# Performance work log

Measured on AMD Instinct MI355X. Metric: run time of the kernel, lower is better.

## Reference

```python
import jax, jax.numpy as jnp
import numpy as np

B, T, D = 4, 2048, 1024
N_HEAD, HEAD_SIZE = 16, 64
MASK_FILL = 1e-9  # faithful to original: masked_fill uses 1e-9, not -inf


def setup_inputs() -> dict:
    key = jax.random.key(0)
    k1, k2, k3 = jax.random.split(key, 3)
    x = jax.random.normal(k1, (B, T, D), dtype=jnp.float32)
    # per-head qkv projection weights, stacked: [n_head, d_model, 3*head_size]
    W_qkv = jax.random.normal(k2, (N_HEAD, D, 3 * HEAD_SIZE), dtype=jnp.float32) * (D ** -0.5)
    # output projection [d_model, d_model] (x @ W_out convention)
    W_out = jax.random.normal(k3, (D, D), dtype=jnp.float32) * (D ** -0.5)
    return {"x": x, "W_qkv": W_qkv, "W_out": W_out}


def reference(x, W_qkv, W_out):
    Bv, Tv, C = x.shape
    # qkv for all heads at once: [B, H, T, 3*head_size]
    qkv = jnp.einsum("btc,hcf->bhtf", x, W_qkv)
    q, k, v = jnp.split(qkv, 3, axis=-1)  # each [B, H, T, head_size]
    # NOTE: original scales by C**-0.5 where C = d_model (not head_size)
    scores = jnp.einsum("bhtd,bhsd->bhts", q, k) * (C ** -0.5)
    causal = jnp.tril(jnp.ones((Tv, Tv), dtype=bool))
    # faithful bug: masked positions set to 1e-9 before softmax (not -inf)
    scores = jnp.where(causal, scores, MASK_FILL)
    attn = jax.nn.softmax(scores, axis=-1)
    out_heads = jnp.einsum("bhts,bhsd->bhtd", attn, v)  # [B, H, T, head_size]
    mha = out_heads.transpose(0, 2, 1, 3).reshape(Bv, Tv, C)  # concat heads
    return mha @ W_out
```

## Files before the change

### kernel.cpp

```cpp
#include <hip/hip_runtime.h>

typedef unsigned short u16;
typedef __attribute__((ext_vector_type(8))) short short8;
typedef __attribute__((ext_vector_type(4))) short short4v;
typedef __attribute__((ext_vector_type(4))) float f32x4;

#define B_  4
#define T_  2048
#define D_  1024
#define H_  16
#define HS_ 64
#define M_    (B_ * T_)
#define NQKV_ (H_ * 3 * HS_)
#define NTILE_ (T_ / 64)
#define LOG2E_ 1.44269504088896340736f

__device__ __forceinline__ u16 f2bf(float f) {
  union { float f; unsigned u; } v; v.f = f;
  unsigned u = v.u;
  return (u16)((u + 0x7FFFu + ((u >> 16) & 1u)) >> 16);
}
__device__ __forceinline__ float bf2f(u16 h) {
  union { unsigned u; float f; } v; v.u = ((unsigned)h) << 16; return v.f;
}
__device__ __forceinline__ unsigned pkbf(float lo, float hi) {
  unsigned r;
  asm("v_cvt_pk_bf16_f32 %0, %1, %2" : "=v"(r) : "v"(lo), "v"(hi));
  return r;
}
__device__ __forceinline__ float exp2fast(float x) {
  float r;
  asm("v_exp_f32 %0, %1" : "=v"(r) : "v"(x));
  return r;
}
__device__ __forceinline__ void gload16(const u16* g, u16* l) {
  __builtin_amdgcn_global_load_lds(
      (const __attribute__((address_space(1))) void*)g,
      (__attribute__((address_space(3))) void*)l, 16, 0, 0);
}

__global__ void k_cvt_x(const float* __restrict__ x, u16* __restrict__ o, int n4) {
  int i = blockIdx.x * 256 + threadIdx.x;
  if (i < n4) {
    float4 v = ((const float4*)x)[i];
    short4v d;
    d[0] = (short)f2bf(v.x); d[1] = (short)f2bf(v.y);
    d[2] = (short)f2bf(v.z); d[3] = (short)f2bf(v.w);
    ((short4v*)o)[i] = d;
  }
}

__global__ void k_transpose_cvt(const float* __restrict__ in, u16* __restrict__ out,
                                int R, int C, long sIn, long sOut) {
  __shared__ float tile[32][33];
  int h = blockIdx.z;
  const float* src = in + (long)h * sIn;
  u16* dst = out + (long)h * sOut;
  int r0 = blockIdx.y * 32, c0 = blockIdx.x * 32;
  int tx = threadIdx.x, ty = threadIdx.y;
  #pragma unroll
  for (int i = 0; i < 32; i += 8) {
    int r = r0 + ty + i, c = c0 + tx;
    tile[ty + i][tx] = (r < R && c < C) ? src[(long)r * C + c] : 0.f;
  }
  __syncthreads();
  #pragma unroll
  for (int i = 0; i < 32; i += 8) {
    int c = c0 + ty + i, r = r0 + tx;
    if (c < C && r < R) dst[(long)c * R + r] = f2bf(tile[tx][ty + i]);
  }
}

template<int MODE>
__global__ __launch_bounds__(256) void k_gemm(
    const u16* __restrict__ A, const u16* __restrict__ Bt,
    u16* __restrict__ Oq, u16* __restrict__ Ok, u16* __restrict__ Ov,
    float* __restrict__ Of, int K) {
  __shared__ __align__(16) u16 As[128 * 32];
  __shared__ __align__(16) u16 Bs[128 * 32];
  int mt = blockIdx.x, nt = blockIdx.y;
  int tid = threadIdx.x;
  int wid = tid >> 6, lane = tid & 63;
  int lr = lane & 15, lg = lane >> 4;
  int mw = (wid >> 1) * 64, nw = (wid & 1) * 64;
  int c0chunk = wid * 128 + lane;
  int row0 = c0chunk >> 2,      q0 = c0chunk & 3;
  int row1 = (c0chunk + 64) >> 2, q1 = (c0chunk + 64) & 3;
  const u16* Arow0 = A  + (long)(mt * 128 + row0) * K + q0 * 8;
  const u16* Arow1 = A  + (long)(mt * 128 + row1) * K + q1 * 8;
  const u16* Brow0 = Bt + (long)(nt * 128 + row0) * K + q0 * 8;
  const u16* Brow1 = Bt + (long)(nt * 128 + row1) * K + q1 * 8;
  u16* ldsA0 = As + (wid * 128) * 8;
  u16* ldsA1 = As + (wid * 128 + 64) * 8;
  u16* ldsB0 = Bs + (wid * 128) * 8;
  u16* ldsB1 = Bs + (wid * 128 + 64) * 8;
  f32x4 acc[4][4] = {};
  for (int k0 = 0; k0 < K; k0 += 32) {
    __syncthreads();
    gload16(Arow0 + k0, ldsA0);
    gload16(Arow1 + k0, ldsA1);
    gload16(Brow0 + k0, ldsB0);
    gload16(Brow1 + k0, ldsB1);
    __syncthreads();
    short8 af[4], bf[4];
    #pragma unroll
    for (int i = 0; i < 4; i++)
      af[i] = *(const short8*)(As + (mw + i * 16 + lr) * 32 + lg * 8);
    #pragma unroll
    for (int i = 0; i < 4; i++)
      bf[i] = *(const short8*)(Bs + (nw + i * 16 + lr) * 32 + lg * 8);
    #pragma unroll
    for (int i = 0; i < 4; i++)
      #pragma unroll
      for (int j = 0; j < 4; j++)
        acc[i][j] = __builtin_amdgcn_mfma_f32_16x16x32_bf16(af[i], bf[j], acc[i][j], 0, 0, 0);
  }
  if constexpr (MODE == 0) {
    __shared__ __align__(16) u16 Cs[128 * 128];
    #pragma unroll
    for (int j = 0; j < 4; j++) {
      int fbase = (nt * 128 + nw + j * 16) % 192;
      float sc = (fbase < 64) ? (0.03125f * LOG2E_) : 1.0f;
      #pragma unroll
      for (int i = 0; i < 4; i++) {
        int row = mw + i * 16 + lg * 4;
        int col = nw + j * 16 + lr;
        #pragma unroll
        for (int r = 0; r < 4; r++)
          Cs[(row + r) * 128 + col] = f2bf(acc[i][j][r] * sc);
      }
    }
    __syncthreads();
    #pragma unroll
    for (int p5 = 0; p5 < 8; p5++) {
      int idx = p5 * 2048 + tid * 8;
      int row = idx >> 7, col = idx & 127;
      short8 v = *(const short8*)(Cs + row * 128 + col);
      int m = mt * 128 + row;
      int n0 = nt * 128 + col;
      int b = m >> 11, t = m & (T_ - 1);
      int h = n0 / 192, f = n0 % 192;
      long o = (((long)(b * H_ + h)) * T_ + t) * HS_;
      u16* dst = (f < 64) ? (Oq + o + f) : (f < 128) ? (Ok + o + f - 64) : (Ov + o + f - 128);
      *(short8*)dst = v;
    }
  } else {
    #pragma unroll
    for (int i = 0; i < 4; i++) {
      #pragma unroll
      for (int j = 0; j < 4; j++) {
        int mbase = mt * 128 + mw + i * 16 + lg * 4;
        int n     = nt * 128 + nw + j * 16 + lr;
        #pragma unroll
        for (int r = 0; r < 4; r++)
          Of[(long)(mbase + r) * D_ + n] = acc[i][j][r];
      }
    }
  }
}

__global__ void k_transpose_v(const u16* __restrict__ V, u16* __restrict__ Vp,
                              float* __restrict__ Partial) {
  __shared__ u16 tile[64][65];
  __shared__ float psum[4][64];
  int bh = blockIdx.z;
  int jt = blockIdx.x;
  int t0 = jt * 64;
  int tx = threadIdx.x & 63, ty = threadIdx.x >> 6;
  const u16* src = V + (long)bh * T_ * HS_;
  u16* dtile = Vp + (((long)bh * NTILE_) + jt) * 64 * 64;
  #pragma unroll
  for (int i = 0; i < 64; i += 4)
    tile[ty + i][tx] = src[(long)(t0 + ty + i) * HS_ + tx];
  __syncthreads();
  int pos = ((tx >> 2) & 3) * 16 + ((tx >> 4) & 3) * 4 + (tx & 3);
  #pragma unroll
  for (int i = 0; i < 64; i += 4)
    dtile[(ty + i) * 64 + pos] = tile[tx][ty + i];
  float s = 0.f;
  #pragma unroll
  for (int i = 0; i < 16; i++)
    s += bf2f(tile[ty * 16 + i][tx]);
  psum[ty][tx] = s;
  __syncthreads();
  if (threadIdx.x < 64)
    Partial[((long)bh * NTILE_ + jt) * HS_ + threadIdx.x] =
        psum[0][threadIdx.x] + psum[1][threadIdx.x] + psum[2][threadIdx.x] + psum[3][threadIdx.x];
}

__global__ void k_vscan(const float* __restrict__ Partial, float* __restrict__ Suf) {
  int bh = blockIdx.x;
  int d = threadIdx.x;
  const float* Pb = Partial + (long)bh * NTILE_ * HS_;
  float* Sb = Suf + (long)bh * (NTILE_ + 1) * HS_;
  float acc = 0.f;
  Sb[NTILE_ * HS_ + d] = 0.f;
  for (int j = NTILE_ - 1; j >= 0; j--) {
    acc += Pb[j * HS_ + d];
    Sb[j * HS_ + d] = acc;
  }
}

__global__ __launch_bounds__(512, 2) void k_attn(
    const u16* __restrict__ Q, const u16* __restrict__ Kc,
    const u16* __restrict__ Vp, const float* __restrict__ Suf,
    u16* __restrict__ Mha) {
  __shared__ __align__(16) u16 Ks[2][64 * 64];
  __shared__ __align__(16) u16 Vs[2][64 * 64];
  int bh = blockIdx.x;
  int xp = blockIdx.y;
  int b = bh >> 4, h = bh & 15;
  int tid = threadIdx.x, wid = tid >> 6, lane = tid & 63;
  int lr = lane & 15, lg = lane >> 4;
  const u16* Qb = Q  + (long)bh * T_ * HS_;
  const u16* Kb = Kc + (long)bh * T_ * HS_;
  const u16* Vb = Vp + (long)bh * T_ * HS_;
  union U8 { unsigned u[4]; short8 s; };
  const short8 vone = { (short)0x3F80, (short)0x3F80, (short)0x3F80, (short)0x3F80,
                        (short)0x3F80, (short)0x3F80, (short)0x3F80, (short)0x3F80 };
  int srow = tid >> 3;
  int schunk = (tid & 7) ^ (srow & 7);
  const u16* kSrc = Kb + srow * 64 + schunk * 8;
  const u16* vSrc = Vb + srow * 64 + schunk * 8;
  const int r7 = lr & 7;
  const int kc0 = (lg ^ r7) << 3, kc1 = ((4 + lg) ^ r7) << 3;
  const int vc0 = ((2 * lg) ^ r7) << 3, vc1 = ((2 * lg + 1) ^ r7) << 3;

  #pragma unroll 1
  for (int half = 0; half < 2; half++) {
    int st = half ? (7 - xp) : xp;
    int q0w = st * 256 + wid * 32;
    short8 qf[2][2];
    #pragma unroll
    for (int g = 0; g < 2; g++) {
      const u16* qp = Qb + (long)(q0w + g * 16 + lr) * HS_;
      qf[g][0] = *(const short8*)(qp + lg * 8);
      qf[g][1] = *(const short8*)(qp + 32 + lg * 8);
    }
    f32x4 accO[2][4] = {};
    f32x4 accL[2] = {};
    const int blkJ = 4 * st + 3;
    const int myJ  = 4 * st + (wid >> 1);
    gload16(kSrc, &Ks[0][wid * 512]);
    gload16(vSrc, &Vs[0][wid * 512]);
    __syncthreads();
    for (int jt = 0; jt <= blkJ; jt++) {
      int cur = jt & 1;
      if (jt < blkJ) {
        long off = (long)(jt + 1) * 4096;
        gload16(kSrc + off, &Ks[cur ^ 1][wid * 512]);
        gload16(vSrc + off, &Vs[cur ^ 1][wid * 512]);
      }
      if (jt <= myJ) {
        int j0 = jt * 64;
        const bool diag = (jt == myJ);
        const u16* Kl = Ks[cur];
        const u16* Vl = Vs[cur];
        f32x4 s4[2][4];
        #pragma unroll
        for (int fn = 0; fn < 4; fn++) {
          const u16* krow = Kl + (fn * 16 + lr) * 64;
          short8 kb0 = *(const short8*)(krow + kc0);
          short8 kb1 = *(const short8*)(krow + kc1);
          #pragma unroll
          for (int g = 0; g < 2; g++) {
            f32x4 z = {};
            z = __builtin_amdgcn_mfma_f32_16x16x32_bf16(kb0, qf[g][0], z, 0, 0, 0);
            z = __builtin_amdgcn_mfma_f32_16x16x32_bf16(kb1, qf[g][1], z, 0, 0, 0);
            s4[g][fn] = z;
          }
        }
        U8 pa[2][2];
        #pragma unroll
        for (int g = 0; g < 2; g++) {
          int qrow = q0w + g * 16 + lr;
          float p[4][4];
          #pragma unroll
          for (int fn = 0; fn < 4; fn++) {
            #pragma unroll
            for (int r = 0; r < 4; r++) {
              float v = s4[g][fn][r];
              if (diag) {
                int s = j0 + fn * 16 + lg * 4 + r;
                v = (s <= qrow) ? v : 0.0f;
              }
              p[fn][r] = exp2fast(v);
            }
          }
          pa[g][0].u[0] = pkbf(p[0][0], p[0][1]); pa[g][0].u[1] = pkbf(p[0][2], p[0][3]);
          pa[g][0].u[2] = pkbf(p[1][0], p[1][1]); pa[g][0].u[3] = pkbf(p[1][2], p[1][3]);
          pa[g][1].u[0] = pkbf(p[2][0], p[2][1]); pa[g][1].u[1] = pkbf(p[2][2], p[2][3]);
          pa[g][1].u[2] = pkbf(p[3][0], p[3][1]); pa[g][1].u[3] = pkbf(p[3][2], p[3][3]);
          accL[g] = __builtin_amdgcn_mfma_f32_16x16x32_bf16(pa[g][0].s, vone, accL[g], 0, 0, 0);
          accL[g] = __builtin_amdgcn_mfma_f32_16x16x32_bf16(pa[g][1].s, vone, accL[g], 0, 0, 0);
        }
        #pragma unroll
        for (int fd = 0; fd < 4; fd++) {
          const u16* vrow = Vl + (fd * 16 + lr) * 64;
          U8 vb0, vb1;
          vb0.s = *(const short8*)(vrow + vc0);
          vb1.s = *(const short8*)(vrow + vc1);
          #pragma unroll
          for (int g = 0; g < 2; g++) {
            accO[g][fd] = __builtin_amdgcn_mfma_f32_16x16x32_bf16(pa[g][0].s, vb0.s, accO[g][fd], 0, 0, 0);
            accO[g][fd] = __builtin_amdgcn_mfma_f32_16x16x32_bf16(pa[g][1].s, vb1.s, accO[g][fd], 0, 0, 0);
          }
        }
      }
      __syncthreads();
    }
    int nmask = T_ - (myJ + 1) * 64;
    const float* sufp = Suf + ((long)bh * (NTILE_ + 1) + (myJ + 1)) * HS_;
    float sufv[4];
    #pragma unroll
    for (int fd = 0; fd < 4; fd++) sufv[fd] = sufp[fd * 16 + lr];
    #pragma unroll
    for (int g = 0; g < 2; g++) {
      #pragma unroll
      for (int fd = 0; fd < 4; fd++) {
        #pragma unroll
        for (int r = 0; r < 4; r++) {
          int trow = q0w + g * 16 + lg * 4 + r;
          float o = (accO[g][fd][r] + sufv[fd]) / (accL[g][r] + (float)nmask);
          Mha[((long)(b * T_ + trow)) * D_ + h * HS_ + fd * 16 + lr] = f2bf(o);
        }
      }
    }
  }
}

extern "C" void kernel_launch(void* const* d_in, const int* in_sizes, int n_in,
                              void* d_out, int out_size, void* d_ws, size_t ws_size,
                              hipStream_t stream) {
  const float* x    = (const float*)d_in[0];
  const float* wqkv = (const float*)d_in[1];
  const float* wout = (const float*)d_in[2];
  float* out = (float*)d_out;

  char* p = (char*)d_ws;
  u16* Xb    = (u16*)p; p += (size_t)M_ * D_ * 2;
  u16* WqkvT = (u16*)p; p += (size_t)NQKV_ * D_ * 2;
  u16* WoutT = (u16*)p; p += (size_t)D_ * D_ * 2;
  u16* Qw  = (u16*)p; p += (size_t)B_ * H_ * T_ * HS_ * 2;
  u16* Kw  = (u16*)p; p += (size_t)B_ * H_ * T_ * HS_ * 2;
  u16* Vw  = (u16*)p; p += (size_t)B_ * H_ * T_ * HS_ * 2;
  u16* Vpw = (u16*)p; p += (size_t)B_ * H_ * T_ * HS_ * 2;
  u16* Mha = (u16*)p; p += (size_t)M_ * D_ * 2;
  float* Suf = (float*)p; p += (size_t)B_ * H_ * (NTILE_ + 1) * HS_ * 4;
  float* Part = (float*)p; p += (size_t)B_ * H_ * NTILE_ * HS_ * 4;

  k_cvt_x<<<dim3(M_ * D_ / 4 / 256), dim3(256), 0, stream>>>(x, Xb, M_ * D_ / 4);
  k_transpose_cvt<<<dim3(192 / 32, D_ / 32, H_), dim3(32, 8), 0, stream>>>(
      wqkv, WqkvT, D_, 192, (long)D_ * 192, (long)192 * D_);
  k_transpose_cvt<<<dim3(D_ / 32, D_ / 32, 1), dim3(32, 8), 0, stream>>>(
      wout, WoutT, D_, D_, 0, 0);
  k_gemm<0><<<dim3(M_ / 128, NQKV_ / 128), dim3(256), 0, stream>>>(
      Xb, WqkvT, Qw, Kw, Vw, nullptr, D_);
  k_transpose_v<<<dim3(T_ / 64, 1, B_ * H_), dim3(256), 0, stream>>>(Vw, Vpw, Part);
  k_vscan<<<dim3(B_ * H_), dim3(64), 0, stream>>>(Part, Suf);
  k_attn<<<dim3(B_ * H_, T_ / 256 / 2), dim3(512), 0, stream>>>(Qw, Kw, Vpw, Suf, Mha);
  k_gemm<1><<<dim3(M_ / 128, D_ / 128), dim3(256), 0, stream>>>(
      Mha, WoutT, nullptr, nullptr, nullptr, out, D_);
}
```

Baseline: 187.1 us.

## Double GEMM K-tile to 64 with XOR-swizzled LDS layout and shared smem

The bf16 GEMM kernel now loads 64-wide K tiles per barrier pair instead of 32, which halves the number of synchronizations per output tile. The LDS layout is XOR-swizzled on 16-byte chunks by row to avoid bank conflicts on the MFMA fragment reads. The epilogue staging buffer aliases the same shared allocation behind an added barrier, so total LDS use stays flat despite the larger tiles. The trade-off is more address computation and more in-flight loads per thread.

```diff
diff --git a/kernel.cpp b/kernel.cpp
--- a/kernel.cpp
+++ b/kernel.cpp
@@ -76,47 +76,54 @@
     const u16* __restrict__ A, const u16* __restrict__ Bt,
     u16* __restrict__ Oq, u16* __restrict__ Ok, u16* __restrict__ Ov,
     float* __restrict__ Of, int K) {
-  __shared__ __align__(16) u16 As[128 * 32];
-  __shared__ __align__(16) u16 Bs[128 * 32];
+  __shared__ __align__(16) u16 smem[128 * 128];
+  u16* As = smem;
+  u16* Bs = smem + 128 * 64;
   int mt = blockIdx.x, nt = blockIdx.y;
   int tid = threadIdx.x;
   int wid = tid >> 6, lane = tid & 63;
   int lr = lane & 15, lg = lane >> 4;
   int mw = (wid >> 1) * 64, nw = (wid & 1) * 64;
-  int c0chunk = wid * 128 + lane;
-  int row0 = c0chunk >> 2,      q0 = c0chunk & 3;
-  int row1 = (c0chunk + 64) >> 2, q1 = (c0chunk + 64) & 3;
-  const u16* Arow0 = A  + (long)(mt * 128 + row0) * K + q0 * 8;
-  const u16* Arow1 = A  + (long)(mt * 128 + row1) * K + q1 * 8;
-  const u16* Brow0 = Bt + (long)(nt * 128 + row0) * K + q0 * 8;
-  const u16* Brow1 = Bt + (long)(nt * 128 + row1) * K + q1 * 8;
-  u16* ldsA0 = As + (wid * 128) * 8;
-  u16* ldsA1 = As + (wid * 128 + 64) * 8;
-  u16* ldsB0 = Bs + (wid * 128) * 8;
-  u16* ldsB1 = Bs + (wid * 128 + 64) * 8;
+  const u16* srcA[4]; const u16* srcB[4];
+  u16* dstA[4]; u16* dstB[4];
+  #pragma unroll
+  for (int l = 0; l < 4; l++) {
+    int c = l * 256 + wid * 64 + lane;
+    int r = c >> 3, q = c & 7;
+    int qs = q ^ (r & 7);
+    srcA[l] = A  + (long)(mt * 128 + r) * K + qs * 8;
+    srcB[l] = Bt + (long)(nt * 128 + r) * K + qs * 8;
+    dstA[l] = As + (l * 256 + wid * 64) * 8;
+    dstB[l] = Bs + (l * 256 + wid * 64) * 8;
+  }
+  const int rsw = (lr & 7);
   f32x4 acc[4][4] = {};
-  for (int k0 = 0; k0 < K; k0 += 32) {
+  for (int k0 = 0; k0 < K; k0 += 64) {
     __syncthreads();
-    gload16(Arow0 + k0, ldsA0);
-    gload16(Arow1 + k0, ldsA1);
-    gload16(Brow0 + k0, ldsB0);
-    gload16(Brow1 + k0, ldsB1);
+    #pragma unroll
+    for (int l = 0; l < 4; l++) gload16(srcA[l] + k0, dstA[l]);
+    #pragma unroll
+    for (int l = 0; l < 4; l++) gload16(srcB[l] + k0, dstB[l]);
     __syncthreads();
-    short8 af[4], bf[4];
-    #pragma unroll
-    for (int i = 0; i < 4; i++)
-      af[i] = *(const short8*)(As + (mw + i * 16 + lr) * 32 + lg * 8);
-    #pragma unroll
-    for (int i = 0; i < 4; i++)
-      bf[i] = *(const short8*)(Bs + (nw + i * 16 + lr) * 32 + lg * 8);
-    #pragma unroll
-    for (int i = 0; i < 4; i++)
-      #pragma unroll
-      for (int j = 0; j < 4; j++)
-        acc[i][j] = __builtin_amdgcn_mfma_f32_16x16x32_bf16(af[i], bf[j], acc[i][j], 0, 0, 0);
-  }
+    #pragma unroll
+    for (int kk = 0; kk < 2; kk++) {
+      short8 af[4], bf[4];
+      #pragma unroll
+      for (int i = 0; i < 4; i++)
+        af[i] = *(const short8*)(As + (mw + i * 16 + lr) * 64 + (((kk * 4 + lg) ^ rsw) << 3));
+      #pragma unroll
+      for (int i = 0; i < 4; i++)
+        bf[i] = *(const short8*)(Bs + (nw + i * 16 + lr) * 64 + (((kk * 4 + lg) ^ rsw) << 3));
+      #pragma unroll
+      for (int i = 0; i < 4; i++)
+        #pragma unroll
+        for (int j = 0; j < 4; j++)
+          acc[i][j] = __builtin_amdgcn_mfma_f32_16x16x32_bf16(af[i], bf[j], acc[i][j], 0, 0, 0);
+    }
+  }
+  __syncthreads();
   if constexpr (MODE == 0) {
-    __shared__ __align__(16) u16 Cs[128 * 128];
+    u16* Cs = smem;
     #pragma unroll
     for (int j = 0; j < 4; j++) {
       int fbase = (nt * 128 + nw + j * 16) % 192;
```

Result: faster. 169.9 us (-9.2%).
